# Optimization experiments

Measured on AMD Instinct MI355X. Metric: run time of the kernel, lower is better.

Reference implementation:

```python
import jax, jax.numpy as jnp
import numpy as np

# graph constants
B, V, CG, K, H, IN = 4, 6250, 25000, 3, 64, 2
NUM_LIT = B * 2 * V          # 50_000 literal nodes
NUM_CLS = B * CG             # 100_000 clause nodes
E = K * NUM_CLS              # 300_000 (l2c, c2l) edge pairs
NUM_ROUND = 3
DEMON = float(np.sqrt(H))    # self.demon = sqrt(hidden_size)


def setup_inputs() -> dict:
    key = jax.random.key(0)
    ks = jax.random.split(key, 12)
    rng = np.random.default_rng(0)
    # each clause has K literal endpoints; edges stay inside their own graph
    cls_idx = np.repeat(np.arange(NUM_CLS), K)
    g = cls_idx // CG
    lit_idx = g * 2 * V + rng.integers(0, 2 * V, size=E)

    def lin(k, fi, fo):
        return (jax.random.normal(k, (fi, fo), jnp.float32) / np.sqrt(fi)).astype(jnp.float32)

    return {
        "feat_l2c": jax.random.normal(ks[0], (E, IN), jnp.float32),
        "feat_c2l": jax.random.normal(ks[1], (E, IN), jnp.float32),
        "lit_idx": jnp.asarray(lit_idx, jnp.int32),
        "cls_idx": jnp.asarray(cls_idx, jnp.int32),
        "W_l2c_init": lin(ks[2], IN, H), "b_l2c_init": jnp.zeros((H,), jnp.float32),
        "W_c2l_init": lin(ks[3], IN, H), "b_c2l_init": jnp.zeros((H,), jnp.float32),
        "msgl_W": (jax.random.normal(ks[4], (3, H, H), jnp.float32) / np.sqrt(H)).astype(jnp.float32),
        "msgl_b": jnp.zeros((3, H), jnp.float32),
        "merge_W0": lin(ks[5], 2 * H, H), "merge_b0": jnp.zeros((H,), jnp.float32),
        "merge_Wr": (jax.random.normal(ks[6], (2, H, H), jnp.float32) / np.sqrt(H)).astype(jnp.float32),
        "merge_br": jnp.zeros((2, H), jnp.float32),
        "msgc_W": (jax.random.normal(ks[7], (3, H, H), jnp.float32) / np.sqrt(H)).astype(jnp.float32),
        "msgc_b": jnp.zeros((3, H), jnp.float32),
        "ro_W": (jax.random.normal(ks[8], (2, H, H), jnp.float32) / np.sqrt(H)).astype(jnp.float32),
        "ro_b": jnp.zeros((2, H), jnp.float32),
        "ro_W2": lin(ks[9], H, 1), "ro_b2": jnp.zeros((1,), jnp.float32),
    }


def _mlp3(x, W, b):  # 3-layer MLP, ReLU between layers (num_fc = 3)
    x = jax.nn.relu(x @ W[0] + b[0])
    x = jax.nn.relu(x @ W[1] + b[1])
    return x @ W[2] + b[2]


def reference(feat_l2c, feat_c2l, lit_idx, cls_idx,
              W_l2c_init, b_l2c_init, W_c2l_init, b_c2l_init,
              msgl_W, msgl_b, merge_W0, merge_b0, merge_Wr, merge_br,
              msgc_W, msgc_b, ro_W, ro_b, ro_W2, ro_b2):
    # init edge embeddings (l2c_init / c2l_init linear layers)
    h_l2c = feat_l2c @ W_l2c_init + b_l2c_init   # [E, H]
    h_c2l = feat_c2l @ W_c2l_init + b_c2l_init   # [E, H]

    for _ in range(NUM_ROUND):
        # literal update: aggregate incoming c2l messages, exclude self edge (BP-style)
        agg_l = jax.ops.segment_sum(h_c2l, lit_idx, num_segments=NUM_LIT)   # [NUM_LIT, H]
        m = _mlp3((agg_l[lit_idx] - h_c2l) / DEMON, msgl_W, msgl_b)          # [E, H]
        x = jax.nn.relu(jnp.concatenate([m, h_l2c], axis=-1) @ merge_W0 + merge_b0)
        x = jax.nn.relu(x @ merge_Wr[0] + merge_br[0])
        h_l2c = x @ merge_Wr[1] + merge_br[1]                                # l2c_merge_update
        # clause update
        agg_c = jax.ops.segment_sum(h_l2c, cls_idx, num_segments=NUM_CLS)   # [NUM_CLS, H]
        h_c2l = _mlp3((agg_c[cls_idx] - h_l2c) / DEMON, msgc_W, msgc_b)

    # u_add_e_sum with zero node feats == scatter-add edge emb to dst;
    # literal nodes only receive c2l edges
    l_emb = jax.ops.segment_sum(h_c2l, lit_idx, num_segments=NUM_LIT)        # [NUM_LIT, H]
    # segment_reduce(num_variable*2, ..., 'mean') over per-graph literal blocks (uniform sizes)
    l_mean = l_emb.reshape(B, 2 * V, H).mean(axis=1)                          # [B, H]
    x = jax.nn.relu(l_mean @ ro_W[0] + ro_b[0])
    x = jax.nn.relu(x @ ro_W[1] + ro_b[1])
    return jax.nn.sigmoid(x @ ro_W2 + ro_b2).squeeze(-1)                      # [B]
```

## Files before the change

kernel.cpp:

```cpp
#include <hip/hip_runtime.h>
#include <hip/hip_bf16.h>
#include <stdint.h>

#define EDGES   300000
#define NLIT    50000
#define NGRAPH  4
#define EPG     75000
#define HDIM    64

#define OFF_HL2C   0
#define OFF_HC2L   38400000
#define OFF_AGG    76800000
#define OFF_WT     89600000
#define OFF_ROACC  89681920
#define OFF_CNT    89682944
#define OFF_CSROFF 89882944
#define OFF_CURSOR 90082948
#define OFF_EIDX   90282948
#define OFF_BSUM   91482948
#define OFF_BBASE  91484000

#define WT_TOTAL    40960
#define WT_CLS_ELEM 28672

#define LIT_WBYTES (7 * 8192)
#define CLS_WBYTES (3 * 8192)
#define EPB3       512
#define GRID_EDGE  ((EDGES + EPB3 - 1) / EPB3)

#define SCAN_BLOCKS ((NLIT + 255) / 256)

typedef __attribute__((ext_vector_type(8)))  short          s16x8;
typedef __attribute__((ext_vector_type(8)))  unsigned short u16x8;
typedef __attribute__((ext_vector_type(4)))  unsigned short u16x4;
typedef __attribute__((ext_vector_type(4)))  float          f32x4;
typedef __attribute__((ext_vector_type(16))) float          f32x16;

__device__ __forceinline__ f32x16 mfma32(s16x8 a, s16x8 b, f32x16 c) {
    return __builtin_amdgcn_mfma_f32_32x32x16_bf16(a, b, c, 0, 0, 0);
}
__device__ __forceinline__ float bf2f(unsigned short s) {
    union { unsigned int u; float f; } v; v.u = ((unsigned int)s) << 16; return v.f;
}
__device__ __forceinline__ unsigned short f2bf(float f) {
    union { __hip_bfloat16 b; unsigned short s; } v;
    v.b = __float2bfloat16(f);
    return v.s;
}
__device__ __forceinline__ unsigned pk2(float a, float b) {
    return (unsigned)f2bf(a) | ((unsigned)f2bf(b) << 16);
}

__device__ __forceinline__ void layer32(const char* __restrict__ unitBase,
                                        const float* __restrict__ biasL,
                                        const s16x8 (&bin)[4], f32x16 (&acc)[2],
                                        int eL, int hi)
{
#pragma unroll
    for (int t = 0; t < 2; ++t)
#pragma unroll
        for (int g = 0; g < 4; ++g) {
            f32x4 bv = *(const f32x4*)(biasL + 32 * t + 8 * g + 4 * hi);
#pragma unroll
            for (int r = 0; r < 4; ++r) acc[t][4 * g + r] = bv[r];
        }
#pragma unroll
    for (int kb = 0; kb < 4; ++kb)
#pragma unroll
        for (int t = 0; t < 2; ++t) {
            int row = 32 * t + eL;
            s16x8 a = *(const s16x8*)(unitBase + row * 128 +
                                      ((32 * kb + 16 * hi) ^ ((row & 7) << 4)));
            acc[t] = mfma32(a, bin[kb], acc[t]);
        }
}

template<bool RELU>
__device__ __forceinline__ void relayout32(f32x16 (&acc)[2], s16x8 (&bout)[4],
                                           int bpidx, int hi)
{
    if (RELU) {
#pragma unroll
        for (int t = 0; t < 2; ++t)
#pragma unroll
            for (int i = 0; i < 16; ++i) acc[t][i] = fmaxf(acc[t][i], 0.f);
    }
#pragma unroll
    for (int kb = 0; kb < 4; ++kb) {
        int m0 = 2 * kb, m1 = 2 * kb + 1;
        int t0 = m0 >> 2, g0 = m0 & 3, t1 = m1 >> 2, g1 = m1 & 3;
        unsigned A0 = pk2(acc[t0][4 * g0 + 0], acc[t0][4 * g0 + 1]);
        unsigned A1 = pk2(acc[t0][4 * g0 + 2], acc[t0][4 * g0 + 3]);
        unsigned B0 = pk2(acc[t1][4 * g1 + 0], acc[t1][4 * g1 + 1]);
        unsigned B1 = pk2(acc[t1][4 * g1 + 2], acc[t1][4 * g1 + 3]);
        unsigned pA0 = (unsigned)__builtin_amdgcn_ds_bpermute(bpidx, (int)A0);
        unsigned pA1 = (unsigned)__builtin_amdgcn_ds_bpermute(bpidx, (int)A1);
        unsigned pB0 = (unsigned)__builtin_amdgcn_ds_bpermute(bpidx, (int)B0);
        unsigned pB1 = (unsigned)__builtin_amdgcn_ds_bpermute(bpidx, (int)B1);
        union { unsigned w[4]; s16x8 v; } u;
        u.w[0] = hi ? pB0 : A0;
        u.w[1] = hi ? pB1 : A1;
        u.w[2] = hi ? B0 : pA0;
        u.w[3] = hi ? B1 : pA1;
        bout[kb] = u.v;
    }
}

__device__ __forceinline__ void store32(const f32x16 (&acc)[2],
                                        unsigned short* __restrict__ dst, int hi)
{
#pragma unroll
    for (int t = 0; t < 2; ++t)
#pragma unroll
        for (int g = 0; g < 4; ++g) {
            u16x4 p;
#pragma unroll
            for (int r = 0; r < 4; ++r) p[r] = f2bf(acc[t][4 * g + r]);
            *(u16x4*)(dst + 32 * t + 8 * g + 4 * hi) = p;
        }
}

__global__ __launch_bounds__(256) void prep_weights(
    const float* __restrict__ msgl_W, const float* __restrict__ merge_W0,
    const float* __restrict__ merge_Wr, const float* __restrict__ msgc_W,
    unsigned short* __restrict__ wT)
{
    int gid = blockIdx.x * 256 + threadIdx.x;
    if (gid >= WT_TOTAL) return;
    int unit = gid >> 12;
    int o = (gid >> 6) & 63;
    int csw = gid & 63;
    int i = csw ^ ((o & 7) << 3);
    float v;
    if (unit < 3)       v = msgl_W[unit * 4096 + i * 64 + o];
    else if (unit < 5)  v = merge_W0[((unit - 3) * 64 + i) * 64 + o];
    else if (unit < 7)  v = merge_Wr[(unit - 5) * 4096 + i * 64 + o];
    else                v = msgc_W[(unit - 7) * 4096 + i * 64 + o];
    wT[gid] = f2bf(v);
}

__global__ __launch_bounds__(256) void csr_hist(const int* __restrict__ lit_idx,
                                                int* __restrict__ cnt)
{
    int e = blockIdx.x * 256 + threadIdx.x;
    if (e < EDGES) atomicAdd(&cnt[lit_idx[e]], 1);
}

__global__ __launch_bounds__(256) void scan1(const int* __restrict__ cnt,
                                             int* __restrict__ bsum)
{
    __shared__ int red[4];
    int i = blockIdx.x * 256 + threadIdx.x;
    int s = (i < NLIT) ? cnt[i] : 0;
#pragma unroll
    for (int off = 1; off < 64; off <<= 1) s += __shfl_xor(s, off, 64);
    if ((threadIdx.x & 63) == 0) red[threadIdx.x >> 6] = s;
    __syncthreads();
    if (threadIdx.x == 0) bsum[blockIdx.x] = red[0] + red[1] + red[2] + red[3];
}

__global__ __launch_bounds__(256) void scan2(const int* __restrict__ bsum,
                                             int* __restrict__ bbase)
{
    __shared__ int tmp[256];
    int t = threadIdx.x;
    int v = (t < SCAN_BLOCKS) ? bsum[t] : 0;
    tmp[t] = v;
    __syncthreads();
#pragma unroll
    for (int off = 1; off < 256; off <<= 1) {
        int add = (t >= off) ? tmp[t - off] : 0;
        __syncthreads();
        tmp[t] += add;
        __syncthreads();
    }
    if (t < SCAN_BLOCKS) bbase[t] = tmp[t] - v;
}

__global__ __launch_bounds__(256) void scan3(const int* __restrict__ cnt,
                                             const int* __restrict__ bbase,
                                             int* __restrict__ off,
                                             int* __restrict__ cursor)
{
    __shared__ int tmp[256];
    int t = threadIdx.x;
    int i = blockIdx.x * 256 + t;
    int v = (i < NLIT) ? cnt[i] : 0;
    tmp[t] = v;
    __syncthreads();
#pragma unroll
    for (int offs = 1; offs < 256; offs <<= 1) {
        int add = (t >= offs) ? tmp[t - offs] : 0;
        __syncthreads();
        tmp[t] += add;
        __syncthreads();
    }
    if (i < NLIT) {
        int ex = bbase[blockIdx.x] + tmp[t] - v;
        off[i] = ex; cursor[i] = ex;
    }
    if (i == NLIT - 1) off[NLIT] = EDGES;
}

__global__ __launch_bounds__(256) void csr_scatter(const int* __restrict__ lit_idx,
                                                   int* __restrict__ cursor,
                                                   int* __restrict__ eidx)
{
    int e = blockIdx.x * 256 + threadIdx.x;
    if (e >= EDGES) return;
    int pos = atomicAdd(&cursor[lit_idx[e]], 1);
    eidx[pos] = e;
}

__global__ __launch_bounds__(256) void aggregate(const unsigned short* __restrict__ h_c2l,
                                                 const int* __restrict__ off,
                                                 const int* __restrict__ eidx,
                                                 float* __restrict__ agg)
{
    int t = threadIdx.x;
    int lane8 = t & 7;
    int lit = blockIdx.x * 32 + (t >> 3);
    if (lit >= NLIT) return;
    int lo = off[lit], hi = off[lit + 1];
    float s[8] = {0, 0, 0, 0, 0, 0, 0, 0};
    int i = lo;
    for (; i + 4 <= hi; i += 4) {
        int e0 = eidx[i], e1 = eidx[i + 1], e2 = eidx[i + 2], e3 = eidx[i + 3];
        u16x8 v0 = *(const u16x8*)(h_c2l + e0 * 64 + lane8 * 8);
        u16x8 v1 = *(const u16x8*)(h_c2l + e1 * 64 + lane8 * 8);
        u16x8 v2 = *(const u16x8*)(h_c2l + e2 * 64 + lane8 * 8);
        u16x8 v3 = *(const u16x8*)(h_c2l + e3 * 64 + lane8 * 8);
#pragma unroll
        for (int j = 0; j < 8; ++j)
            s[j] += (bf2f(v0[j]) + bf2f(v1[j])) + (bf2f(v2[j]) + bf2f(v3[j]));
    }
    for (; i < hi; ++i) {
        int e = eidx[i];
        u16x8 hv = *(const u16x8*)(h_c2l + e * 64 + lane8 * 8);
#pragma unroll
        for (int j = 0; j < 8; ++j) s[j] += bf2f(hv[j]);
    }
    f32x4 a0, a1;
    a0[0] = s[0]; a0[1] = s[1]; a0[2] = s[2]; a0[3] = s[3];
    a1[0] = s[4]; a1[1] = s[5]; a1[2] = s[6]; a1[3] = s[7];
    *(f32x4*)(agg + lit * 64 + lane8 * 8)     = a0;
    *(f32x4*)(agg + lit * 64 + lane8 * 8 + 4) = a1;
}

__global__ __launch_bounds__(256) void init_kernel(
    const float* __restrict__ feat_l2c, const float* __restrict__ feat_c2l,
    const float* __restrict__ W_l2c, const float* __restrict__ b_l2c,
    const float* __restrict__ W_c2l, const float* __restrict__ b_c2l,
    unsigned short* __restrict__ h_l2c, unsigned short* __restrict__ h_c2l)
{
    int gid = blockIdx.x * 256 + threadIdx.x;
    if (gid >= EDGES * 8) return;
    int e = gid >> 3, fo = (gid & 7) << 3;
    float2 fl = *(const float2*)(feat_l2c + e * 2);
    float2 fc = *(const float2*)(feat_c2l + e * 2);

    u16x8 outl, outc;
#pragma unroll
    for (int j = 0; j < 8; ++j) {
        float wl0 = W_l2c[fo + j], wl1 = W_l2c[64 + fo + j];
        float wc0 = W_c2l[fo + j], wc1 = W_c2l[64 + fo + j];
        float vl = fl.x * wl0 + fl.y * wl1 + b_l2c[fo + j];
        float vc = fc.x * wc0 + fc.y * wc1 + b_c2l[fo + j];
        outl[j] = f2bf(vl);
        outc[j] = f2bf(vc);
    }
    *(u16x8*)(h_l2c + e * 64 + fo) = outl;
    *(u16x8*)(h_c2l + e * 64 + fo) = outc;
}

__global__ __launch_bounds__(1024, 4) void lit_update(
    const unsigned short* __restrict__ h_c2l,
    unsigned short* __restrict__ h_l2c,
    const float* __restrict__ agg,
    const int* __restrict__ lit_idx,
    const unsigned short* __restrict__ wT,
    const float* __restrict__ msgl_b,
    const float* __restrict__ merge_b0,
    const float* __restrict__ merge_br)
{
    __shared__ __align__(16) char lds[LIT_WBYTES + 384 * 4];
    int tid = threadIdx.x;
    for (int c = tid; c < LIT_WBYTES / 16; c += 1024)
        *(u16x8*)(lds + c * 16) = *(const u16x8*)(wT + c * 8);
    float* ldsBias = (float*)(lds + LIT_WBYTES);
    if (tid < 384) {
        float v;
        if (tid < 192)      v = msgl_b[tid];
        else if (tid < 256) v = merge_b0[tid - 192];
        else                v = merge_br[tid - 256];
        ldsBias[tid] = v;
    }
    __syncthreads();

    int wv = tid >> 6, lane = tid & 63;
    int eL = lane & 31, hi = lane >> 5;
    int bpidx = (lane ^ 32) << 2;
    int base = blockIdx.x * EPB3 + wv * 32;
    if (base >= EDGES) return;
    int e = base + eL;
    int lit = lit_idx[e];

    s16x8 hfrag[4];
#pragma unroll
    for (int k = 0; k < 4; ++k)
        hfrag[k] = *(const s16x8*)(h_l2c + e * 64 + 16 * k + 8 * hi);

    s16x8 binp[4];
#pragma unroll
    for (int k = 0; k < 4; ++k) {
        int f0 = 16 * k + 8 * hi;
        f32x4 a0 = *(const f32x4*)(agg + lit * 64 + f0);
        f32x4 a1 = *(const f32x4*)(agg + lit * 64 + f0 + 4);
        u16x8 hv = *(const u16x8*)(h_c2l + e * 64 + f0);
        s16x8 b;
#pragma unroll
        for (int j = 0; j < 4; ++j) b[j]     = (short)f2bf((a0[j] - bf2f(hv[j]))     * 0.125f);
#pragma unroll
        for (int j = 0; j < 4; ++j) b[4 + j] = (short)f2bf((a1[j] - bf2f(hv[4 + j])) * 0.125f);
        binp[k] = b;
    }

    f32x16 acc[2];
    s16x8 bf[4];
    layer32(lds,            ldsBias,       binp, acc, eL, hi);
    relayout32<true >(acc, bf, bpidx, hi);
    layer32(lds + 8192,     ldsBias + 64,  bf, acc, eL, hi);
    relayout32<true >(acc, bf, bpidx, hi);
    layer32(lds + 2 * 8192, ldsBias + 128, bf, acc, eL, hi);
    relayout32<false>(acc, bf, bpidx, hi);

#pragma unroll
    for (int t = 0; t < 2; ++t)
#pragma unroll
        for (int g = 0; g < 4; ++g) {
            f32x4 bv = *(const f32x4*)(ldsBias + 192 + 32 * t + 8 * g + 4 * hi);
#pragma unroll
            for (int r = 0; r < 4; ++r) acc[t][4 * g + r] = bv[r];
        }
#pragma unroll
    for (int kb = 0; kb < 8; ++kb) {
        const char* ub = lds + (3 + (kb >> 2)) * 8192;
        s16x8 bop = (kb < 4) ? bf[kb] : hfrag[kb - 4];
#pragma unroll
        for (int t = 0; t < 2; ++t) {
            int row = 32 * t + eL;
            s16x8 a = *(const s16x8*)(ub + row * 128 +
                                      ((32 * (kb & 3) + 16 * hi) ^ ((row & 7) << 4)));
            acc[t] = mfma32(a, bop, acc[t]);
        }
    }
    relayout32<true>(acc, bf, bpidx, hi);
    layer32(lds + 5 * 8192, ldsBias + 256, bf, acc, eL, hi);
    relayout32<true>(acc, bf, bpidx, hi);
    layer32(lds + 6 * 8192, ldsBias + 320, bf, acc, eL, hi);

    store32(acc, h_l2c + e * 64, hi);
}

__global__ __launch_bounds__(1024, 4) void clause_update(
    const unsigned short* __restrict__ h_l2c,
    unsigned short* __restrict__ h_c2l,
    const unsigned short* __restrict__ msgcT,
    const float* __restrict__ msgc_b)
{
    __shared__ __align__(16) char lds[CLS_WBYTES + 192 * 4];
    int tid = threadIdx.x;
    for (int c = tid; c < CLS_WBYTES / 16; c += 1024)
        *(u16x8*)(lds + c * 16) = *(const u16x8*)(msgcT + c * 8);
    float* ldsBias = (float*)(lds + CLS_WBYTES);
    if (tid < 192) ldsBias[tid] = msgc_b[tid];
    __syncthreads();

    int wv = tid >> 6, lane = tid & 63;
    int eL = lane & 31, hi = lane >> 5;
    int bpidx = (lane ^ 32) << 2;
    int base = blockIdx.x * EPB3 + wv * 32;
    if (base >= EDGES) return;
    int e = base + eL;

    int c3 = (e / 3) * 3;
    int d = e - c3;
    int e1 = c3 + (d == 0 ? 1 : 0);
    int e2 = c3 + (d == 2 ? 1 : 2);

    s16x8 binp[4];
#pragma unroll
    for (int k = 0; k < 4; ++k) {
        int f0 = 16 * k + 8 * hi;
        u16x8 h1 = *(const u16x8*)(h_l2c + e1 * 64 + f0);
        u16x8 h2 = *(const u16x8*)(h_l2c + e2 * 64 + f0);
        s16x8 b;
#pragma unroll
        for (int j = 0; j < 8; ++j)
            b[j] = (short)f2bf((bf2f(h1[j]) + bf2f(h2[j])) * 0.125f);
        binp[k] = b;
    }

    f32x16 acc[2];
    s16x8 bf[4];
    layer32(lds,            ldsBias,       binp, acc, eL, hi);
    relayout32<true>(acc, bf, bpidx, hi);
    layer32(lds + 8192,     ldsBias + 64,  bf, acc, eL, hi);
    relayout32<true>(acc, bf, bpidx, hi);
    layer32(lds + 2 * 8192, ldsBias + 128, bf, acc, eL, hi);

    store32(acc, h_c2l + e * 64, hi);
}

__global__ __launch_bounds__(256) void readout_sum(
    const unsigned short* __restrict__ h_c2l, float* __restrict__ ro_acc)
{
    __shared__ float lsum[32][64];
    int g = blockIdx.x >> 6, chunk = blockIdx.x & 63;
    int t = threadIdx.x;
    int fg = t & 7, el = t >> 3;
    float s[8] = {0, 0, 0, 0, 0, 0, 0, 0};
    for (int idx = chunk * 32 + el; idx < EPG; idx += 2048) {
        u16x8 hv = *(const u16x8*)(h_c2l + (g * EPG + idx) * 64 + fg * 8);
#pragma unroll
        for (int j = 0; j < 8; ++j) s[j] += bf2f(hv[j]);
    }
#pragma unroll
    for (int j = 0; j < 8; ++j) lsum[el][fg * 8 + j] = s[j];
    __syncthreads();
    if (t < 64) {
        float tot = 0.f;
#pragma unroll 8
        for (int r = 0; r < 32; ++r) tot += lsum[r][t];
        atomicAdd(&ro_acc[g * 64 + t], tot);
    }
}

__global__ __launch_bounds__(256) void readout_mlp(
    const float* __restrict__ ro_acc, const float* __restrict__ ro_W,
    const float* __restrict__ ro_b, const float* __restrict__ ro_W2,
    const float* __restrict__ ro_b2, float* __restrict__ out)
{
    __shared__ float xb[NGRAPH][HDIM];
    __shared__ float yb[NGRAPH][HDIM];
    int g = threadIdx.x >> 6;
    int j = threadIdx.x & 63;
    xb[g][j] = ro_acc[g * HDIM + j] * (1.0f / 12500.0f);
    __syncthreads();
    float a = ro_b[j];
#pragma unroll 8
    for (int k = 0; k < HDIM; ++k) a += xb[g][k] * ro_W[k * HDIM + j];
    a = fmaxf(a, 0.0f);
    yb[g][j] = a;
    __syncthreads();
    float a2 = ro_b[HDIM + j];
#pragma unroll 8
    for (int k = 0; k < HDIM; ++k) a2 += yb[g][k] * ro_W[4096 + k * HDIM + j];
    a2 = fmaxf(a2, 0.0f);
    float p = a2 * ro_W2[j];
#pragma unroll
    for (int off = 32; off > 0; off >>= 1) p += __shfl_down(p, off, 64);
    if (j == 0) out[g] = 1.0f / (1.0f + expf(-(p + ro_b2[0])));
}

extern "C" void kernel_launch(void* const* d_in, const int* in_sizes, int n_in,
                              void* d_out, int out_size, void* d_ws, size_t ws_size,
                              hipStream_t stream)
{
    const float* feat_l2c = (const float*)d_in[0];
    const float* feat_c2l = (const float*)d_in[1];
    const int*   lit_idx  = (const int*)d_in[2];
    const float* W_l2c    = (const float*)d_in[4];
    const float* b_l2c    = (const float*)d_in[5];
    const float* W_c2l    = (const float*)d_in[6];
    const float* b_c2l    = (const float*)d_in[7];
    const float* msgl_W   = (const float*)d_in[8];
    const float* msgl_b   = (const float*)d_in[9];
    const float* merge_W0 = (const float*)d_in[10];
    const float* merge_b0 = (const float*)d_in[11];
    const float* merge_Wr = (const float*)d_in[12];
    const float* merge_br = (const float*)d_in[13];
    const float* msgc_W   = (const float*)d_in[14];
    const float* msgc_b   = (const float*)d_in[15];
    const float* ro_W     = (const float*)d_in[16];
    const float* ro_b     = (const float*)d_in[17];
    const float* ro_W2    = (const float*)d_in[18];
    const float* ro_b2    = (const float*)d_in[19];

    char* ws = (char*)d_ws;
    unsigned short* h_l2c  = (unsigned short*)(ws + OFF_HL2C);
    unsigned short* h_c2l  = (unsigned short*)(ws + OFF_HC2L);
    float*          agg    = (float*)(ws + OFF_AGG);
    unsigned short* wT     = (unsigned short*)(ws + OFF_WT);
    float*          ro_acc = (float*)(ws + OFF_ROACC);
    int*            cnt    = (int*)(ws + OFF_CNT);
    int*            csroff = (int*)(ws + OFF_CSROFF);
    int*            cursor = (int*)(ws + OFF_CURSOR);
    int*            eidx   = (int*)(ws + OFF_EIDX);
    int*            bsum   = (int*)(ws + OFF_BSUM);
    int*            bbase  = (int*)(ws + OFF_BBASE);

    hipMemsetAsync(cnt, 0, NLIT * sizeof(int), stream);
    hipMemsetAsync(ro_acc, 0, NGRAPH * 64 * sizeof(float), stream);

    prep_weights<<<(WT_TOTAL + 255) / 256, 256, 0, stream>>>(msgl_W, merge_W0, merge_Wr, msgc_W, wT);

    csr_hist<<<(EDGES + 255) / 256, 256, 0, stream>>>(lit_idx, cnt);
    scan1<<<SCAN_BLOCKS, 256, 0, stream>>>(cnt, bsum);
    scan2<<<1, 256, 0, stream>>>(bsum, bbase);
    scan3<<<SCAN_BLOCKS, 256, 0, stream>>>(cnt, bbase, csroff, cursor);
    csr_scatter<<<(EDGES + 255) / 256, 256, 0, stream>>>(lit_idx, cursor, eidx);

    init_kernel<<<EDGES * 8 / 256, 256, 0, stream>>>(feat_l2c, feat_c2l, W_l2c, b_l2c,
                                                     W_c2l, b_c2l, h_l2c, h_c2l);
    for (int r = 0; r < 3; ++r) {
        aggregate<<<(NLIT + 31) / 32, 256, 0, stream>>>(h_c2l, csroff, eidx, agg);
        lit_update<<<GRID_EDGE, 1024, 0, stream>>>(h_c2l, h_l2c, agg, lit_idx, wT,
                                                   msgl_b, merge_b0, merge_br);
        clause_update<<<GRID_EDGE, 1024, 0, stream>>>(h_l2c, h_c2l, wT + WT_CLS_ELEM, msgc_b);
    }
    readout_sum<<<256, 256, 0, stream>>>(h_c2l, ro_acc);
    readout_mlp<<<1, 256, 0, stream>>>(ro_acc, ro_W, ro_b, ro_W2, ro_b2, (float*)d_out);
}
```

Baseline: 352.9 us.

## Hold MLP weights in registers with persistent waves; split literal update

```diff
diff --git a/kernel.cpp b/kernel.cpp
--- a/kernel.cpp
+++ b/kernel.cpp
@@ -19,14 +19,19 @@
 #define OFF_EIDX   90282948
 #define OFF_BSUM   91482948
 #define OFF_BBASE  91484000
+#define OFF_M      91500032
+#define WS_NEED_M  (OFF_M + 38400000ULL)
 
 #define WT_TOTAL    40960
 #define WT_CLS_ELEM 28672
 
 #define LIT_WBYTES (7 * 8192)
-#define CLS_WBYTES (3 * 8192)
-#define EPB3       512
-#define GRID_EDGE  ((EDGES + EPB3 - 1) / EPB3)
+#define EPB2       256
+#define GRID_FUSED ((EDGES + EPB2 - 1) / EPB2)
+
+#define NWCH       (EDGES / 32)
+#define REG_GRID   512
+#define REG_WAVES  (REG_GRID * 4)
 
 #define SCAN_BLOCKS ((NLIT + 255) / 256)
 
@@ -51,28 +56,36 @@
     return (unsigned)f2bf(a) | ((unsigned)f2bf(b) << 16);
 }
 
-__device__ __forceinline__ void layer32(const char* __restrict__ unitBase,
-                                        const float* __restrict__ biasL,
-                                        const s16x8 (&bin)[4], f32x16 (&acc)[2],
-                                        int eL, int hi)
+__device__ __forceinline__ void layer32r(const s16x8 (&wA)[8],
+                                         const float* __restrict__ biasG,
+                                         const s16x8 (&bin)[4], f32x16 (&acc)[2],
+                                         int hi)
 {
 #pragma unroll
     for (int t = 0; t < 2; ++t)
 #pragma unroll
         for (int g = 0; g < 4; ++g) {
-            f32x4 bv = *(const f32x4*)(biasL + 32 * t + 8 * g + 4 * hi);
+            f32x4 bv = *(const f32x4*)(biasG + 32 * t + 8 * g + 4 * hi);
 #pragma unroll
             for (int r = 0; r < 4; ++r) acc[t][4 * g + r] = bv[r];
         }
+    __builtin_amdgcn_s_setprio(1);
 #pragma unroll
     for (int kb = 0; kb < 4; ++kb)
 #pragma unroll
-        for (int t = 0; t < 2; ++t) {
-            int row = 32 * t + eL;
-            s16x8 a = *(const s16x8*)(unitBase + row * 128 +
-                                      ((32 * kb + 16 * hi) ^ ((row & 7) << 4)));
-            acc[t] = mfma32(a, bin[kb], acc[t]);
-        }
+        for (int t = 0; t < 2; ++t)
+            acc[t] = mfma32(wA[kb * 2 + t], bin[kb], acc[t]);
+    __builtin_amdgcn_s_setprio(0);
+}
+
+__device__ __forceinline__ void load_wunit(const unsigned short* __restrict__ wu,
+                                           int eL, int hi, s16x8 (&wA)[8])
+{
+#pragma unroll
+    for (int kb = 0; kb < 4; ++kb)
+#pragma unroll
+        for (int t = 0; t < 2; ++t)
+            wA[kb * 2 + t] = *(const s16x8*)(wu + (32 * t + eL) * 64 + 32 * kb + 16 * hi);
 }
 
 template<bool RELU>
@@ -129,8 +142,7 @@
     if (gid >= WT_TOTAL) return;
     int unit = gid >> 12;
     int o = (gid >> 6) & 63;
-    int csw = gid & 63;
-    int i = csw ^ ((o & 7) << 3);
+    int i = gid & 63;
     float v;
     if (unit < 3)       v = msgl_W[unit * 4096 + i * 64 + o];
     else if (unit < 5)  v = merge_W0[((unit - 3) * 64 + i) * 64 + o];
@@ -273,7 +285,173 @@
     *(u16x8*)(h_c2l + e * 64 + fo) = outc;
 }
 
-__global__ __launch_bounds__(1024, 4) void lit_update(
+__global__ __launch_bounds__(256, 2) void lit_msg(
+    const unsigned short* __restrict__ h_c2l,
+    const float* __restrict__ agg,
+    const int* __restrict__ lit_idx,
+    const unsigned short* __restrict__ wT,
+    const float* __restrict__ msgl_b,
+    unsigned short* __restrict__ m_ws)
+{
+    int tid = threadIdx.x;
+    int wv = tid >> 6, lane = tid & 63;
+    int eL = lane & 31, hi = lane >> 5;
+    int bpidx = (lane ^ 32) << 2;
+
+    s16x8 w0[8], w1[8], w2[8];
+    load_wunit(wT,            eL, hi, w0);
+    load_wunit(wT + 4096,     eL, hi, w1);
+    load_wunit(wT + 2 * 4096, eL, hi, w2);
+
+    int wid = blockIdx.x * 4 + wv;
+    for (int w = wid; w < NWCH; w += REG_WAVES) {
+        int e = w * 32 + eL;
+        int lit = lit_idx[e];
+
+        s16x8 binp[4];
+#pragma unroll
+        for (int k = 0; k < 4; ++k) {
+            int f0 = 16 * k + 8 * hi;
+            f32x4 a0 = *(const f32x4*)(agg + lit * 64 + f0);
+            f32x4 a1 = *(const f32x4*)(agg + lit * 64 + f0 + 4);
+            u16x8 hv = *(const u16x8*)(h_c2l + e * 64 + f0);
+            s16x8 b;
+#pragma unroll
+            for (int j = 0; j < 4; ++j) b[j]     = (short)f2bf((a0[j] - bf2f(hv[j]))     * 0.125f);
+#pragma unroll
+            for (int j = 0; j < 4; ++j) b[4 + j] = (short)f2bf((a1[j] - bf2f(hv[4 + j])) * 0.125f);
+            binp[k] = b;
+        }
+
+        f32x16 acc[2];
+        s16x8 bf[4];
+        layer32r(w0, msgl_b,       binp, acc, hi);
+        relayout32<true >(acc, bf, bpidx, hi);
+        layer32r(w1, msgl_b + 64,  bf, acc, hi);
+        relayout32<true >(acc, bf, bpidx, hi);
+        layer32r(w2, msgl_b + 128, bf, acc, hi);
+        relayout32<false>(acc, bf, bpidx, hi);
+
+        unsigned short* mb = m_ws + w * 2048;
+#pragma unroll
+        for (int kb = 0; kb < 4; ++kb)
+            *(u16x8*)(mb + kb * 512 + lane * 8) = *(const u16x8*)&bf[kb];
+    }
+}
+
+__global__ __launch_bounds__(256, 2) void lit_merge(
+    unsigned short* __restrict__ h_l2c,
+    const unsigned short* __restrict__ m_ws,
+    const unsigned short* __restrict__ wT,
+    const float* __restrict__ merge_b0,
+    const float* __restrict__ merge_br)
+{
+    int tid = threadIdx.x;
+    int wv = tid >> 6, lane = tid & 63;
+    int eL = lane & 31, hi = lane >> 5;
+    int bpidx = (lane ^ 32) << 2;
+
+    s16x8 wm[8], wh[8], wr0[8], wr1[8];
+    load_wunit(wT + 3 * 4096, eL, hi, wm);
+    load_wunit(wT + 4 * 4096, eL, hi, wh);
+    load_wunit(wT + 5 * 4096, eL, hi, wr0);
+    load_wunit(wT + 6 * 4096, eL, hi, wr1);
+
+    int wid = blockIdx.x * 4 + wv;
+    for (int w = wid; w < NWCH; w += REG_WAVES) {
+        int e = w * 32 + eL;
+
+        s16x8 mf[4], hfrag[4];
+        const unsigned short* mb = m_ws + w * 2048;
+#pragma unroll
+        for (int kb = 0; kb < 4; ++kb)
+            mf[kb] = *(const s16x8*)(mb + kb * 512 + lane * 8);
+#pragma unroll
+        for (int k = 0; k < 4; ++k)
+            hfrag[k] = *(const s16x8*)(h_l2c + e * 64 + 16 * k + 8 * hi);
+
+        f32x16 acc[2];
+#pragma unroll
+        for (int t = 0; t < 2; ++t)
+#pragma unroll
+            for (int g = 0; g < 4; ++g) {
+                f32x4 bv = *(const f32x4*)(merge_b0 + 32 * t + 8 * g + 4 * hi);
+#pragma unroll
+                for (int r = 0; r < 4; ++r) acc[t][4 * g + r] = bv[r];
+            }
+        __builtin_amdgcn_s_setprio(1);
+#pragma unroll
+        for (int kb = 0; kb < 4; ++kb)
+#pragma unroll
+            for (int t = 0; t < 2; ++t)
+                acc[t] = mfma32(wm[kb * 2 + t], mf[kb], acc[t]);
+#pragma unroll
+        for (int kb = 0; kb < 4; ++kb)
+#pragma unroll
+            for (int t = 0; t < 2; ++t)
+                acc[t] = mfma32(wh[kb * 2 + t], hfrag[kb], acc[t]);
+        __builtin_amdgcn_s_setprio(0);
+
+        s16x8 bf[4];
+        relayout32<true>(acc, bf, bpidx, hi);
+        layer32r(wr0, merge_br,      bf, acc, hi);
+        relayout32<true>(acc, bf, bpidx, hi);
+        layer32r(wr1, merge_br + 64, bf, acc, hi);
+
+        store32(acc, h_l2c + e * 64, hi);
+    }
+}
+
+__global__ __launch_bounds__(256, 2) void clause_reg(
+    const unsigned short* __restrict__ h_l2c,
+    unsigned short* __restrict__ h_c2l,
+    const unsigned short* __restrict__ wT,
+    const float* __restrict__ msgc_b)
+{
+    int tid = threadIdx.x;
+    int wv = tid >> 6, lane = tid & 63;
+    int eL = lane & 31, hi = lane >> 5;
+    int bpidx = (lane ^ 32) << 2;
+
+    s16x8 w0[8], w1[8], w2[8];
+    load_wunit(wT + WT_CLS_ELEM,            eL, hi, w0);
+    load_wunit(wT + WT_CLS_ELEM + 4096,     eL, hi, w1);
+    load_wunit(wT + WT_CLS_ELEM + 2 * 4096, eL, hi, w2);
+
+    int wid = blockIdx.x * 4 + wv;
+    for (int w = wid; w < NWCH; w += REG_WAVES) {
+        int e = w * 32 + eL;
+        int c3 = (e / 3) * 3;
+        int d = e - c3;
+        int e1 = c3 + (d == 0 ? 1 : 0);
+        int e2 = c3 + (d == 2 ? 1 : 2);
+
+        s16x8 binp[4];
+#pragma unroll
+        for (int k = 0; k < 4; ++k) {
+            int f0 = 16 * k + 8 * hi;
+            u16x8 h1 = *(const u16x8*)(h_l2c + e1 * 64 + f0);
+            u16x8 h2 = *(const u16x8*)(h_l2c + e2 * 64 + f0);
+            s16x8 b;
+#pragma unroll
+            for (int j = 0; j < 8; ++j)
+                b[j] = (short)f2bf((bf2f(h1[j]) + bf2f(h2[j])) * 0.125f);
+            binp[k] = b;
+        }
+
+        f32x16 acc[2];
+        s16x8 bf[4];
+        layer32r(w0, msgc_b,       binp, acc, hi);
+        relayout32<true>(acc, bf, bpidx, hi);
+        layer32r(w1, msgc_b + 64,  bf, acc, hi);
+        relayout32<true>(acc, bf, bpidx, hi);
+        layer32r(w2, msgc_b + 128, bf, acc, hi);
+
+        store32(acc, h_c2l + e * 64, hi);
+    }
+}
+
+__global__ __launch_bounds__(512, 4) void lit_fused(
     const unsigned short* __restrict__ h_c2l,
     unsigned short* __restrict__ h_l2c,
     const float* __restrict__ agg,
@@ -285,8 +463,11 @@
 {
     __shared__ __align__(16) char lds[LIT_WBYTES + 384 * 4];
     int tid = threadIdx.x;
-    for (int c = tid; c < LIT_WBYTES / 16; c += 1024)
-        *(u16x8*)(lds + c * 16) = *(const u16x8*)(wT + c * 8);
+    for (int c = tid; c < LIT_WBYTES / 16; c += 512) {
+        u16x8 v = *(const u16x8*)(wT + c * 8);
+        int u = c >> 9, row = (c >> 3) & 63, slot = c & 7;
+        *(u16x8*)(lds + u * 8192 + row * 128 + ((slot * 16) ^ ((row & 7) << 4))) = v;
+    }
     float* ldsBias = (float*)(lds + LIT_WBYTES);
     if (tid < 384) {
         float v;
@@ -300,7 +481,7 @@
     int wv = tid >> 6, lane = tid & 63;
     int eL = lane & 31, hi = lane >> 5;
     int bpidx = (lane ^ 32) << 2;
-    int base = blockIdx.x * EPB3 + wv * 32;
+    int base = blockIdx.x * EPB2 + wv * 32;
     if (base >= EDGES) return;
     int e = base + eL;
     int lit = lit_idx[e];
@@ -327,11 +508,34 @@
 
     f32x16 acc[2];
     s16x8 bf[4];
-    layer32(lds,            ldsBias,       binp, acc, eL, hi);
+#define LDS_LAYER(UB, BIASOFF, BIN)                                                   \
+    {                                                                                 \
+        const char* ub = lds + (UB) * 8192;                                           \
+        const float* bl = ldsBias + (BIASOFF);                                        \
+        _Pragma("unroll")                                                             \
+        for (int t = 0; t < 2; ++t)                                                   \
+            _Pragma("unroll")                                                         \
+            for (int g = 0; g < 4; ++g) {                                             \
+                f32x4 bv = *(const f32x4*)(bl + 32 * t + 8 * g + 4 * hi);             \
+                _Pragma("unroll")                                                     \
+                for (int r = 0; r < 4; ++r) acc[t][4 * g + r] = bv[r];                \
+            }                                                                         \
+        _Pragma("unroll")                                                             \
+        for (int kb = 0; kb < 4; ++kb)                                                \
+            _Pragma("unroll")                                                         \
+            for (int t = 0; t < 2; ++t) {                                             \
+                int row = 32 * t + eL;                                                \
+                s16x8 a = *(const s16x8*)(ub + row * 128 +                            \
+                                          ((32 * kb + 16 * hi) ^ ((row & 7) << 4)));  \
+                acc[t] = mfma32(a, (BIN)[kb], acc[t]);                                \
+            }                                                                         \
+    }
+
+    LDS_LAYER(0, 0,   binp);
     relayout32<true >(acc, bf, bpidx, hi);
-    layer32(lds + 8192,     ldsBias + 64,  bf, acc, eL, hi);
+    LDS_LAYER(1, 64,  bf);
     relayout32<true >(acc, bf, bpidx, hi);
-    layer32(lds + 2 * 8192, ldsBias + 128, bf, acc, eL, hi);
+    LDS_LAYER(2, 128, bf);
     relayout32<false>(acc, bf, bpidx, hi);
 
 #pragma unroll
@@ -355,61 +559,12 @@
         }
     }
     relayout32<true>(acc, bf, bpidx, hi);
-    layer32(lds + 5 * 8192, ldsBias + 256, bf, acc, eL, hi);
+    LDS_LAYER(5, 256, bf);
     relayout32<true>(acc, bf, bpidx, hi);
-    layer32(lds + 6 * 8192, ldsBias + 320, bf, acc, eL, hi);
+    LDS_LAYER(6, 320, bf);
+#undef LDS_LAYER
 
     store32(acc, h_l2c + e * 64, hi);
-}
-
-__global__ __launch_bounds__(1024, 4) void clause_update(
-    const unsigned short* __restrict__ h_l2c,
-    unsigned short* __restrict__ h_c2l,
-    const unsigned short* __restrict__ msgcT,
-    const float* __restrict__ msgc_b)
-{
-    __shared__ __align__(16) char lds[CLS_WBYTES + 192 * 4];
-    int tid = threadIdx.x;
-    for (int c = tid; c < CLS_WBYTES / 16; c += 1024)
-        *(u16x8*)(lds + c * 16) = *(const u16x8*)(msgcT + c * 8);
-    float* ldsBias = (float*)(lds + CLS_WBYTES);
-    if (tid < 192) ldsBias[tid] = msgc_b[tid];
-    __syncthreads();
-
-    int wv = tid >> 6, lane = tid & 63;
-    int eL = lane & 31, hi = lane >> 5;
-    int bpidx = (lane ^ 32) << 2;
-    int base = blockIdx.x * EPB3 + wv * 32;
-    if (base >= EDGES) return;
-    int e = base + eL;
-
-    int c3 = (e / 3) * 3;
-    int d = e - c3;
-    int e1 = c3 + (d == 0 ? 1 : 0);
-    int e2 = c3 + (d == 2 ? 1 : 2);
-
-    s16x8 binp[4];
-#pragma unroll
-    for (int k = 0; k < 4; ++k) {
-        int f0 = 16 * k + 8 * hi;
-        u16x8 h1 = *(const u16x8*)(h_l2c + e1 * 64 + f0);
-        u16x8 h2 = *(const u16x8*)(h_l2c + e2 * 64 + f0);
-        s16x8 b;
-#pragma unroll
-        for (int j = 0; j < 8; ++j)
-            b[j] = (short)f2bf((bf2f(h1[j]) + bf2f(h2[j])) * 0.125f);
-        binp[k] = b;
-    }
-
-    f32x16 acc[2];
-    s16x8 bf[4];
-    layer32(lds,            ldsBias,       binp, acc, eL, hi);
-    relayout32<true>(acc, bf, bpidx, hi);
-    layer32(lds + 8192,     ldsBias + 64,  bf, acc, eL, hi);
-    relayout32<true>(acc, bf, bpidx, hi);
-    layer32(lds + 2 * 8192, ldsBias + 128, bf, acc, eL, hi);
-
-    store32(acc, h_c2l + e * 64, hi);
 }
 
 __global__ __launch_bounds__(256) void readout_sum(
@@ -499,6 +654,9 @@
     int*            eidx   = (int*)(ws + OFF_EIDX);
     int*            bsum   = (int*)(ws + OFF_BSUM);
     int*            bbase  = (int*)(ws + OFF_BBASE);
+    unsigned short* m_ws   = (unsigned short*)(ws + OFF_M);
+
+    const bool use_split = (ws_size >= WS_NEED_M);
 
     hipMemsetAsync(cnt, 0, NLIT * sizeof(int), stream);
     hipMemsetAsync(ro_acc, 0, NGRAPH * 64 * sizeof(float), stream);
@@ -515,9 +673,14 @@
                                                      W_c2l, b_c2l, h_l2c, h_c2l);
     for (int r = 0; r < 3; ++r) {
         aggregate<<<(NLIT + 31) / 32, 256, 0, stream>>>(h_c2l, csroff, eidx, agg);
-        lit_update<<<GRID_EDGE, 1024, 0, stream>>>(h_c2l, h_l2c, agg, lit_idx, wT,
-                                                   msgl_b, merge_b0, merge_br);
-        clause_update<<<GRID_EDGE, 1024, 0, stream>>>(h_l2c, h_c2l, wT + WT_CLS_ELEM, msgc_b);
+        if (use_split) {
+            lit_msg<<<REG_GRID, 256, 0, stream>>>(h_c2l, agg, lit_idx, wT, msgl_b, m_ws);
+            lit_merge<<<REG_GRID, 256, 0, stream>>>(h_l2c, m_ws, wT, merge_b0, merge_br);
+        } else {
+            lit_fused<<<GRID_FUSED, 512, 0, stream>>>(h_c2l, h_l2c, agg, lit_idx, wT,
+                                                      msgl_b, merge_b0, merge_br);
+        }
+        clause_reg<<<REG_GRID, 256, 0, stream>>>(h_l2c, h_c2l, wT, msgc_b);
     }
     readout_sum<<<256, 256, 0, stream>>>(h_c2l, ro_acc);
     readout_mlp<<<1, 256, 0, stream>>>(ro_acc, ro_W, ro_b, ro_W2, ro_b2, (float*)d_out);
```

Result: slower. 451.3 us (+27.9%).
